# Optimization experiments

Measured on AMD Instinct MI355X. Metric: run time of the kernel, lower is better.

The kernel has to match this reference:

```python
import jax, jax.numpy as jnp
import numpy as np

N_NODES = 100000
N_EDGES = 3200000
N_GRAPHS = 1024
DIMS = [14, 64, 64, 32, 2]


def _add_self_loops(edge_index, n):
    loop = jnp.arange(n, dtype=edge_index.dtype)
    src = jnp.concatenate([edge_index[0], loop])
    dst = jnp.concatenate([edge_index[1], loop])
    return src, dst


def _gcn_norm(src, dst, n):
    # symmetric normalization D^{-1/2} (A+I) D^{-1/2}; degree from target nodes
    deg = jax.ops.segment_sum(jnp.ones_like(dst, dtype=jnp.float32), dst, num_segments=n)
    dinv = jnp.where(deg > 0, jax.lax.rsqrt(deg), 0.0)
    return dinv[src] * dinv[dst]


def gcn_conv(x, W, b, src, dst, norm, n):
    h = x @ W                          # [N, out] small GEMM first (out <= in here is fine either way)
    msg = h[src] * norm[:, None]       # gather + edge scale  [E+N, out]
    agg = jax.ops.segment_sum(msg, dst, num_segments=n)  # scatter-add
    return agg + b


def setup_inputs() -> dict:
    key = jax.random.key(0)
    ks = jax.random.split(key, 16)
    x = jax.random.normal(ks[0], (N_NODES, DIMS[0]), dtype=jnp.float32)
    edge_index = jax.random.randint(ks[1], (2, N_EDGES), 0, N_NODES, dtype=jnp.int64)
    batch = jnp.sort(jax.random.randint(ks[2], (N_NODES,), 0, N_GRAPHS, dtype=jnp.int64))
    params = {}
    for i in range(4):
        fan_in = DIMS[i]
        params[f"W{i+1}"] = jax.random.normal(ks[3 + 2 * i], (DIMS[i], DIMS[i + 1]), dtype=jnp.float32) / np.sqrt(fan_in)
        params[f"b{i+1}"] = jnp.zeros((DIMS[i + 1],), dtype=jnp.float32)
    return {"x": x, "edge_index": edge_index, "batch": batch, **params}


def reference(x, edge_index, batch, W1, b1, W2, b2, W3, b3, W4, b4):
    n = x.shape[0]
    src, dst = _add_self_loops(edge_index, n)
    norm = _gcn_norm(src, dst, n)
    h = jax.nn.relu(gcn_conv(x, W1, b1, src, dst, norm, n))
    # dropout layers are identity in eval mode
    h = jax.nn.relu(gcn_conv(h, W2, b2, src, dst, norm, n))
    h = jax.nn.relu(gcn_conv(h, W3, b3, src, dst, norm, n))
    h = gcn_conv(h, W4, b4, src, dst, norm, n)
    pooled = jax.ops.segment_max(h, batch, num_segments=N_GRAPHS)  # [G, C]
    pooled = jnp.where(jnp.isfinite(pooled), pooled, 0.0)  # guard empty graphs
    return jax.nn.log_softmax(pooled, axis=-1)
```

## Files before the change

### kernel.cpp

```cpp
#include <hip/hip_runtime.h>
#include <math.h>

#define WAVE 64
#define BINSHIFT 9
#define NPB 512
#define NBLK 512
#define MAXBINS 256
#define BINCAP 17408

typedef int vint4 __attribute__((ext_vector_type(4)));
typedef unsigned int uint;
typedef unsigned char uchar;
typedef __attribute__((ext_vector_type(8))) short bf16x8;
typedef __attribute__((ext_vector_type(4))) float f32x4;

__device__ inline float bflo(uint u) { return __uint_as_float(u << 16); }
__device__ inline float bfhi(uint u) { return __uint_as_float(u & 0xffff0000u); }
__device__ inline uint pack_bf2(float a, float b) {
    uint ua = __float_as_uint(a), ub = __float_as_uint(b);
    uint ra = (ua + 0x7fffu + ((ua >> 16) & 1u)) >> 16;
    uint rb = (ub + 0x7fffu + ((ub >> 16) & 1u)) & 0xffff0000u;
    return ra | rb;
}
__device__ inline ushort bf16r(float f) {
    uint u = __float_as_uint(f);
    u += 0x7fffu + ((u >> 16) & 1u);
    return (ushort)(u >> 16);
}


#if defined(__HIP_DEVICE_COMPILE__) && __has_builtin(__builtin_amdgcn_cvt_pk_f32_fp8) && __has_builtin(__builtin_amdgcn_cvt_pk_fp8_f32)
#define FP8_HW 1
#else
#define FP8_HW 0
#endif

__device__ inline uint fp8_enc1(float x) {
    float cx = fminf(fmaxf(x, -448.f), 448.f);
    uint s = (__float_as_uint(cx) >> 24) & 0x80u;
    float ax = fabsf(cx);
    uint r = __float_as_uint(ax);
    uint keep = r >> 20;
    uint rem = r & 0xFFFFFu;
    keep += (rem > 0x80000u || (rem == 0x80000u && (keep & 1u))) ? 1u : 0u;
    int em = (int)keep - (120 << 3);
    uint sub = (uint)__float2int_rn(ax * 512.f);
    uint v = (ax >= 0.015625f) ? (uint)(em > 0x7E ? 0x7E : em) : sub;
    return s | v;
}
__device__ inline float fp8_dec1(uint b) {
    uint s = (b & 0x80u) << 24;
    uint em = b & 0x7Fu;
    float mag = (em >= 8u)
        ? __uint_as_float((((em >> 3) + 120u) << 23) | ((em & 7u) << 20))
        : (float)em * 0.001953125f;
    return __uint_as_float(s | __float_as_uint(mag));
}

__device__ inline uint fp8x4_enc(float a0, float a1, float a2, float a3) {
#if FP8_HW
    int v = __builtin_amdgcn_cvt_pk_fp8_f32(a0, a1, 0, 0);
    v     = __builtin_amdgcn_cvt_pk_fp8_f32(a2, a3, v, 1);
    return (uint)v;
#else
    return fp8_enc1(a0) | (fp8_enc1(a1) << 8) | (fp8_enc1(a2) << 16) | (fp8_enc1(a3) << 24);
#endif
}
__device__ inline void fp8x4_dec(uint u, float& a0, float& a1, float& a2, float& a3) {
#if FP8_HW
    auto lo = __builtin_amdgcn_cvt_pk_f32_fp8((int)u, 0);
    auto hi = __builtin_amdgcn_cvt_pk_f32_fp8((int)u, 1);
    a0 = lo[0]; a1 = lo[1]; a2 = hi[0]; a3 = hi[1];
#else
    a0 = fp8_dec1(u & 0xffu); a1 = fp8_dec1((u >> 8) & 0xffu);
    a2 = fp8_dec1((u >> 16) & 0xffu); a3 = fp8_dec1(u >> 24);
#endif
}


__global__ __launch_bounds__(1024) void hist_k(const int* __restrict__ ei, int* __restrict__ counts,
                                               int E, int nbins) {
    __shared__ int scnt[MAXBINS];
    int t = threadIdx.x, b = blockIdx.x;
    if (t < nbins) scnt[t] = 0;
    __syncthreads();
    int nq  = E >> 2;
    int qpb = (nq + NBLK - 1) / NBLK;
    int q0 = b * qpb, q1 = min(q0 + qpb, nq);
    for (int q = q0 + t; q < q1; q += 1024) {
        vint4 d4 = __builtin_nontemporal_load(reinterpret_cast<const vint4*>(ei + E + q * 4));
        atomicAdd(&scnt[d4.x >> BINSHIFT], 1);
        atomicAdd(&scnt[d4.y >> BINSHIFT], 1);
        atomicAdd(&scnt[d4.z >> BINSHIFT], 1);
        atomicAdd(&scnt[d4.w >> BINSHIFT], 1);
    }
    if (b == NBLK - 1 && t == 0)
        for (int e = (E & ~3); e < E; ++e) atomicAdd(&scnt[ei[E + e] >> BINSHIFT], 1);
    __syncthreads();
    if (t < nbins) counts[b * nbins + t] = scnt[t];
}


__global__ __launch_bounds__(NBLK) void scan_k(const int* __restrict__ counts, int* __restrict__ prefix,
                                               int* __restrict__ totals, const int* __restrict__ batch,
                                               int* __restrict__ gstart, ushort* __restrict__ padX,
                                               uint* __restrict__ pad8, int nbins, int N, int Gn) {
    __shared__ int sm[NBLK];
    int bin = blockIdx.x, t = threadIdx.x;
    int v = counts[t * nbins + bin];
    sm[t] = v;
    __syncthreads();
    for (int off = 1; off < NBLK; off <<= 1) {
        int x = (t >= off) ? sm[t - off] : 0;
        __syncthreads();
        sm[t] += x;
        __syncthreads();
    }
    prefix[t * nbins + bin] = sm[t] - v;
    if (t == NBLK - 1) totals[bin] = sm[t];
    int gtid = bin * NBLK + t;
    if (gtid < N) {
        int bi = batch[gtid];
        int bp = (gtid == 0) ? -1 : batch[gtid - 1];
        for (int g = bp + 1; g <= bi; ++g) gstart[g] = gtid;
        if (gtid == N - 1)
            for (int g = bi + 1; g <= Gn; ++g) gstart[g] = N;
    }
    if (gtid < 128) padX[gtid] = 0;
    if (gtid < 64)  pad8[gtid] = 0;
}


__global__ __launch_bounds__(1024) void place_k(const int* __restrict__ ei, const int* __restrict__ prefix,
                                                int* __restrict__ binned, int E, int nbins) {
    __shared__ int soff[MAXBINS];
    int t = threadIdx.x, b = blockIdx.x;
    if (t < nbins) soff[t] = prefix[b * nbins + t];
    __syncthreads();
    int nq  = E >> 2;
    int qpb = (nq + NBLK - 1) / NBLK;
    int q0 = b * qpb, q1 = min(q0 + qpb, nq);
    for (int q = q0 + t; q < q1; q += 1024) {
        vint4 s4 = __builtin_nontemporal_load(reinterpret_cast<const vint4*>(ei + q * 4));
        vint4 d4 = __builtin_nontemporal_load(reinterpret_cast<const vint4*>(ei + E + q * 4));
        int bb, p;
        bb = d4.x >> BINSHIFT; p = atomicAdd(&soff[bb], 1);
        if (p < BINCAP) binned[bb * BINCAP + p] = ((d4.x & (NPB - 1)) << 17) | s4.x;
        bb = d4.y >> BINSHIFT; p = atomicAdd(&soff[bb], 1);
        if (p < BINCAP) binned[bb * BINCAP + p] = ((d4.y & (NPB - 1)) << 17) | s4.y;
        bb = d4.z >> BINSHIFT; p = atomicAdd(&soff[bb], 1);
        if (p < BINCAP) binned[bb * BINCAP + p] = ((d4.z & (NPB - 1)) << 17) | s4.z;
        bb = d4.w >> BINSHIFT; p = atomicAdd(&soff[bb], 1);
        if (p < BINCAP) binned[bb * BINCAP + p] = ((d4.w & (NPB - 1)) << 17) | s4.w;
    }
    if (b == NBLK - 1 && t == 0) {
        for (int e = (E & ~3); e < E; ++e) {
            int d = ei[E + e], bb = d >> BINSHIFT;
            int p = atomicAdd(&soff[bb], 1);
            if (p < BINCAP) binned[bb * BINCAP + p] = ((d & (NPB - 1)) << 17) | ei[e];
        }
    }
}


__global__ __launch_bounds__(1024) void bin_sort_k(
    const int* __restrict__ totals, const int* __restrict__ binned, const float* __restrict__ x,
    int* __restrict__ csr, int* __restrict__ deg, int* __restrict__ rowstart,
    float* __restrict__ dinv_g, ushort* __restrict__ xs0b, int N) {
    __shared__ int scnt[NPB];
    __shared__ int sscan[NPB];
    __shared__ int sfill[NPB];
    int bin = blockIdx.x;
    int t   = threadIdx.x;
    int total = totals[bin];
    if (total > BINCAP) total = BINCAP;
    if (t < NPB) { scnt[t] = 0; sfill[t] = 0; }
    __syncthreads();
    const int* gsrc = binned + bin * BINCAP;
    for (int i = t; i < total; i += 1024) atomicAdd(&scnt[gsrc[i] >> 17], 1);
    __syncthreads();
    if (t < NPB) sscan[t] = scnt[t];
    __syncthreads();
    for (int off = 1; off < NPB; off <<= 1) {
        int a = (t < NPB && t >= off) ? sscan[t - off] : 0;
        __syncthreads();
        if (t < NPB) sscan[t] += a;
        __syncthreads();
    }
    int obase = bin * BINCAP;
    for (int i = t; i < total; i += 1024) {
        int rec = gsrc[i], n = rec >> 17;
        int r = atomicAdd(&sfill[n], 1);
        csr[obase + (sscan[n] - scnt[n]) + r] = rec & 0x1FFFF;
    }
    if (t < NPB) {
        int node = (bin << BINSHIFT) + t;
        if (node < N) {
            int c = scnt[t];
            deg[node]      = c;
            rowstart[node] = obase + sscan[t] - c;
            dinv_g[node]   = rsqrtf((float)(c + 1));
        }
    }
    int base = bin << BINSHIFT;
    for (int i = t; i < NPB * 8; i += 1024) {
        int nloc = i >> 3, c2 = i & 7;
        int node = base + nloc;
        if (node < N) {
            float di = rsqrtf((float)(scnt[nloc] + 1));
            int c0 = c2 * 2, c1 = c0 + 1;
            float a = (c0 < 14) ? x[node * 14 + c0] * di : 0.f;
            float b = (c1 < 14) ? x[node * 14 + c1] * di : 0.f;
            reinterpret_cast<uint*>(xs0b)[node * 8 + c2] = pack_bf2(a, b);
        }
    }
}


__global__ __launch_bounds__(256) void agg12_k(
    const ushort* __restrict__ xs, const int* __restrict__ deg, const int* __restrict__ rowstart,
    const int* __restrict__ csr, const float* __restrict__ dinv,
    const float* __restrict__ W1, const float* __restrict__ b1,
    uchar* __restrict__ h1f8, int N) {
    const int G = 4;
    __shared__ float sW1[14 * 64];
    __shared__ float sB1[64];
    int t = threadIdx.x;
    for (int i = t; i < 14 * 64; i += 256) sW1[i] = W1[i];
    if (t < 64) sB1[t] = b1[t];
    __syncthreads();
    int tid  = blockIdx.x * 256 + t;
    int lane = t & (WAVE - 1);
    int wave = tid >> 6;
    int node = wave * (WAVE / G) + lane / G;
    int cg   = lane % G;
    if (node >= N) return;
    int s = rowstart[node];
    int e = s + deg[node];
    float4 acc = {0.f, 0.f, 0.f, 0.f};
    for (int j = s; j < e; j += G) {
        int es = (j + cg < e) ? csr[j + cg] : -1;
#pragma unroll
        for (int k = 0; k < G; ++k) {
            int sk = __shfl(es, k, G);
            uint2 u = *reinterpret_cast<const uint2*>(xs + (long)sk * 16 + (cg << 2));
            acc.x += bflo(u.x); acc.y += bfhi(u.x);
            acc.z += bflo(u.y); acc.w += bfhi(u.y);
        }
    }
    {
        uint2 u = *reinterpret_cast<const uint2*>(xs + (long)node * 16 + (cg << 2));
        acc.x += bflo(u.x); acc.y += bfhi(u.x);
        acc.z += bflo(u.y); acc.w += bfhi(u.y);
    }
    float di = dinv[node];
    float r0 = acc.x * di, r1 = acc.y * di, r2 = acc.z * di, r3 = acc.w * di;
    float rr[16];
#pragma unroll
    for (int k = 0; k < 4; ++k) {
        rr[4 * k + 0] = __shfl(r0, k, G);
        rr[4 * k + 1] = __shfl(r1, k, G);
        rr[4 * k + 2] = __shfl(r2, k, G);
        rr[4 * k + 3] = __shfl(r3, k, G);
    }
    int ob = cg << 4;
    float a[16];
#pragma unroll
    for (int o = 0; o < 16; ++o) a[o] = sB1[ob + o];
#pragma unroll
    for (int c = 0; c < 14; ++c) {
        float rc = rr[c];
#pragma unroll
        for (int o = 0; o < 16; ++o) a[o] += rc * sW1[c * 64 + ob + o];
    }
    uint* orow = reinterpret_cast<uint*>(h1f8 + (long)node * 64 + ob);
#pragma unroll
    for (int o = 0; o < 16; o += 4) {
        float x0 = fmaxf(a[o + 0], 0.f) * di;
        float x1 = fmaxf(a[o + 1], 0.f) * di;
        float x2 = fmaxf(a[o + 2], 0.f) * di;
        float x3 = fmaxf(a[o + 3], 0.f) * di;
        orow[o >> 2] = fp8x4_enc(x0, x1, x2, x3);
    }
}


template <int CO, int G>
__global__ __launch_bounds__(256) void agg2_k(
    const uint* __restrict__ xs, ushort* __restrict__ out,
    const int* __restrict__ deg, const int* __restrict__ rowstart, const int* __restrict__ csr,
    const float* __restrict__ dinv, int N) {
    int tid  = blockIdx.x * blockDim.x + threadIdx.x;
    int lane = threadIdx.x & (WAVE - 1);
    int wave = tid >> 6;
    int node = wave * (WAVE / G) + lane / G;
    int cg   = lane % G;
    if (node >= N) return;
    int s = rowstart[node];
    int e = s + deg[node];
    float4 acc = {0.f, 0.f, 0.f, 0.f};
    for (int j = s; j < e; j += G) {
        int es = (j + cg < e) ? csr[j + cg] : -1;
#pragma unroll
        for (int k = 0; k < G; ++k) {
            int sk = __shfl(es, k, G);
            uint u = xs[(long)sk * G + cg];
            float a0, a1, a2, a3;
            fp8x4_dec(u, a0, a1, a2, a3);
            acc.x += a0; acc.y += a1; acc.z += a2; acc.w += a3;
        }
    }
    {
        uint u = xs[(long)node * G + cg];
        float a0, a1, a2, a3;
        fp8x4_dec(u, a0, a1, a2, a3);
        acc.x += a0; acc.y += a1; acc.z += a2; acc.w += a3;
    }
    float di = dinv[node];
    uint2 o;
    o.x = pack_bf2(acc.x * di, acc.y * di);
    o.y = pack_bf2(acc.z * di, acc.w * di);
    *reinterpret_cast<uint2*>(out + (long)node * CO + (cg << 2)) = o;
}


#define GW 72

__global__ __launch_bounds__(256) void gemm23_k(
    const ushort* __restrict__ inb, const float* __restrict__ W2, const float* __restrict__ b2,
    const float* __restrict__ W3, const float* __restrict__ dinv,
    uchar* __restrict__ outp, int N) {
    __shared__ ushort sW2t[64 * GW];
    __shared__ ushort sW3t[32 * GW];
    __shared__ float  sB2[64];
    __shared__ ushort sH[4][16 * GW];
    __shared__ uchar  sO[4][16 * 32];
    int t = threadIdx.x;
    for (int i = t; i < 64 * 64; i += 256) {
        int k = i >> 6, n = i & 63;
        sW2t[n * GW + k] = bf16r(W2[k * 64 + n]);
    }
    for (int i = t; i < 64 * 32; i += 256) {
        int k = i >> 5, n = i & 31;
        sW3t[n * GW + k] = bf16r(W3[k * 32 + n]);
    }
    if (t < 64) sB2[t] = b2[t];
    __syncthreads();

    int w    = t >> 6;
    int lane = t & 63;
    int m16  = lane & 15;
    int q    = lane >> 4;
    int base = blockIdx.x * 64 + w * 16;

    bf16x8 a0 = *reinterpret_cast<const bf16x8*>(inb + (long)(base + m16) * 64 + q * 8);
    bf16x8 a1 = *reinterpret_cast<const bf16x8*>(inb + (long)(base + m16) * 64 + 32 + q * 8);

    f32x4 acc1[4];
#pragma unroll
    for (int nt = 0; nt < 4; ++nt) {
        f32x4 c = {0.f, 0.f, 0.f, 0.f};
        bf16x8 b0 = *reinterpret_cast<const bf16x8*>(&sW2t[(nt * 16 + m16) * GW + q * 8]);
        bf16x8 b1 = *reinterpret_cast<const bf16x8*>(&sW2t[(nt * 16 + m16) * GW + 32 + q * 8]);
        c = __builtin_amdgcn_mfma_f32_16x16x32_bf16(a0, b0, c, 0, 0, 0);
        c = __builtin_amdgcn_mfma_f32_16x16x32_bf16(a1, b1, c, 0, 0, 0);
        acc1[nt] = c;
    }
    ushort* hT = sH[w];
#pragma unroll
    for (int nt = 0; nt < 4; ++nt) {
        float bb = sB2[nt * 16 + m16];
#pragma unroll
        for (int r = 0; r < 4; ++r) {
            float h = fmaxf(acc1[nt][r] + bb, 0.f);
            hT[(q * 4 + r) * GW + nt * 16 + m16] = bf16r(h);
        }
    }
    __syncthreads();
    bf16x8 a20 = *reinterpret_cast<const bf16x8*>(&hT[m16 * GW + q * 8]);
    bf16x8 a21 = *reinterpret_cast<const bf16x8*>(&hT[m16 * GW + 32 + q * 8]);
    f32x4 acc2[2];
#pragma unroll
    for (int nt = 0; nt < 2; ++nt) {
        f32x4 c = {0.f, 0.f, 0.f, 0.f};
        bf16x8 b0 = *reinterpret_cast<const bf16x8*>(&sW3t[(nt * 16 + m16) * GW + q * 8]);
        bf16x8 b1 = *reinterpret_cast<const bf16x8*>(&sW3t[(nt * 16 + m16) * GW + 32 + q * 8]);
        c = __builtin_amdgcn_mfma_f32_16x16x32_bf16(a20, b0, c, 0, 0, 0);
        c = __builtin_amdgcn_mfma_f32_16x16x32_bf16(a21, b1, c, 0, 0, 0);
        acc2[nt] = c;
    }
    uchar* oT = sO[w];
#pragma unroll
    for (int r = 0; r < 4; ++r) {
        int m = q * 4 + r;
        float di = dinv[min(base + m, N - 1)];
#pragma unroll
        for (int nt = 0; nt < 2; ++nt)
            oT[m * 32 + nt * 16 + m16] = (uchar)fp8_enc1(acc2[nt][r] * di);
    }
    __syncthreads();
    const uint* src = reinterpret_cast<const uint*>(oT);
    uint* dst = reinterpret_cast<uint*>(outp + (long)base * 32);
    dst[lane] = src[lane];
    dst[lane + 64] = src[lane + 64];
}


__global__ __launch_bounds__(256) void agg34_k(
    const uint* __restrict__ xs, const int* __restrict__ deg, const int* __restrict__ rowstart,
    const int* __restrict__ csr, const float* __restrict__ dinv, const float* __restrict__ b3,
    const float* __restrict__ W4, ushort* __restrict__ usb, int N) {
    const int G = 8;
    __shared__ float sW4[64];
    __shared__ float sB3[32];
    int t = threadIdx.x;
    if (t < 64) sW4[t] = W4[t];
    if (t < 32) sB3[t] = b3[t];
    __syncthreads();
    int tid  = blockIdx.x * 256 + t;
    int lane = t & (WAVE - 1);
    int wave = tid >> 6;
    int node = wave * (WAVE / G) + lane / G;
    int cg   = lane % G;
    if (node >= N) return;
    int s = rowstart[node];
    int e = s + deg[node];
    float4 acc = {0.f, 0.f, 0.f, 0.f};
    for (int j = s; j < e; j += G) {
        int es = (j + cg < e) ? csr[j + cg] : -1;
#pragma unroll
        for (int k = 0; k < G; ++k) {
            int sk = __shfl(es, k, G);
            uint u = xs[(long)sk * G + cg];
            float a0, a1, a2, a3;
            fp8x4_dec(u, a0, a1, a2, a3);
            acc.x += a0; acc.y += a1; acc.z += a2; acc.w += a3;
        }
    }
    {
        uint u = xs[(long)node * G + cg];
        float a0, a1, a2, a3;
        fp8x4_dec(u, a0, a1, a2, a3);
        acc.x += a0; acc.y += a1; acc.z += a2; acc.w += a3;
    }
    float di = dinv[node];
    int cb = cg << 2;
    float h0 = fmaxf(acc.x * di + sB3[cb + 0], 0.f);
    float h1 = fmaxf(acc.y * di + sB3[cb + 1], 0.f);
    float h2 = fmaxf(acc.z * di + sB3[cb + 2], 0.f);
    float h3 = fmaxf(acc.w * di + sB3[cb + 3], 0.f);
    float p0 = h0 * sW4[(cb + 0) * 2 + 0] + h1 * sW4[(cb + 1) * 2 + 0]
             + h2 * sW4[(cb + 2) * 2 + 0] + h3 * sW4[(cb + 3) * 2 + 0];
    float p1 = h0 * sW4[(cb + 0) * 2 + 1] + h1 * sW4[(cb + 1) * 2 + 1]
             + h2 * sW4[(cb + 2) * 2 + 1] + h3 * sW4[(cb + 3) * 2 + 1];
#pragma unroll
    for (int o = 4; o >= 1; o >>= 1) {
        p0 += __shfl_xor(p0, o, WAVE);
        p1 += __shfl_xor(p1, o, WAVE);
    }
    if (cg == 0)
        reinterpret_cast<uint*>(usb)[node] = pack_bf2(p0 * di, p1 * di);
}


#define PG 16

__global__ __launch_bounds__(256) void agg4_k(
    const ushort* __restrict__ xs, const int* __restrict__ deg, const int* __restrict__ rowstart,
    const int* __restrict__ csr, const float* __restrict__ dinv, const float* __restrict__ bias,
    float* __restrict__ nodeout, int N) {
    int tid  = blockIdx.x * 256 + threadIdx.x;
    int lane = threadIdx.x & (WAVE - 1);
    int wave = tid >> 6;
    int node = wave * (WAVE / PG) + lane / PG;
    int l    = lane % PG;
    if (node >= N) return;
    int s = rowstart[node];
    int e = s + deg[node];
    float ax = 0.f, ay = 0.f;
    for (int j = s + l; j < e; j += PG) {
        int es = csr[j];
        uint u = *reinterpret_cast<const uint*>(xs + (long)es * 2);
        ax += bflo(u); ay += bfhi(u);
    }
#pragma unroll
    for (int o = PG / 2; o >= 1; o >>= 1) {
        ax += __shfl_xor(ax, o, WAVE);
        ay += __shfl_xor(ay, o, WAVE);
    }
    if (l == 0) {
        uint u = *reinterpret_cast<const uint*>(xs + (long)node * 2);
        ax += bflo(u); ay += bfhi(u);
        float di = dinv[node];
        float2 r;
        r.x = ax * di + bias[0];
        r.y = ay * di + bias[1];
        *reinterpret_cast<float2*>(nodeout + (long)node * 2) = r;
    }
}


__global__ __launch_bounds__(256) void pool_g_k(
    const float* __restrict__ nodeout, const int* __restrict__ gstart,
    float* __restrict__ out, int Gn) {
    int wave = (blockIdx.x * 256 + threadIdx.x) >> 6;
    int lane = threadIdx.x & (WAVE - 1);
    if (wave >= Gn) return;
    int s = gstart[wave], e = gstart[wave + 1];
    float ax = -INFINITY, ay = -INFINITY;
    for (int i = s + lane; i < e; i += WAVE) {
        float2 v = *reinterpret_cast<const float2*>(nodeout + (long)i * 2);
        ax = fmaxf(ax, v.x); ay = fmaxf(ay, v.y);
    }
#pragma unroll
    for (int o = 32; o >= 1; o >>= 1) {
        ax = fmaxf(ax, __shfl_xor(ax, o, WAVE));
        ay = fmaxf(ay, __shfl_xor(ay, o, WAVE));
    }
    if (lane == 0) {
        if (!isfinite(ax)) ax = 0.f;
        if (!isfinite(ay)) ay = 0.f;
        float m = fmaxf(ax, ay);
        float lse = m + logf(expf(ax - m) + expf(ay - m));
        out[wave * 2 + 0] = ax - lse;
        out[wave * 2 + 1] = ay - lse;
    }
}


static inline int agg_blocks(int N, int G) {
    long waves = ((long)N + (WAVE / G) - 1) / (WAVE / G);
    return (int)((waves * WAVE + 255) / 256);
}

extern "C" void kernel_launch(void* const* d_in, const int* in_sizes, int n_in,
                              void* d_out, int out_size, void* d_ws, size_t ws_size,
                              hipStream_t stream) {
    const float* x     = (const float*)d_in[0];
    const int*   ei    = (const int*)d_in[1];
    const int*   batch = (const int*)d_in[2];
    const float* W1 = (const float*)d_in[3];
    const float* b1 = (const float*)d_in[4];
    const float* W2 = (const float*)d_in[5];
    const float* b2 = (const float*)d_in[6];
    const float* W3 = (const float*)d_in[7];
    const float* b3 = (const float*)d_in[8];
    const float* W4 = (const float*)d_in[9];
    const float* b4 = (const float*)d_in[10];
    float* out = (float*)d_out;

    int N  = in_sizes[0] / 14;
    int E  = in_sizes[1] / 2;
    int Gn = out_size / 2;
    int nbins = (N + NPB - 1) >> BINSHIFT;

    char* ws = (char*)d_ws;
    size_t off = 0;
    auto alloc = [&](size_t bytes) -> char* {
        char* p = ws + off;
        off = (off + bytes + 255) & ~(size_t)255;
        return p;
    };
    int*    deg      = (int*)alloc((size_t)N * 4);
    int*    rowstart = (int*)alloc((size_t)N * 4);
    float*  dinv     = (float*)alloc((size_t)N * 4);
    int*    gstart   = (int*)alloc((size_t)(Gn + 1) * 4);
    int*    counts   = (int*)alloc((size_t)NBLK * nbins * 4);
    int*    prefix   = (int*)alloc((size_t)NBLK * nbins * 4);
    int*    totals   = (int*)alloc((size_t)nbins * 4);
    int*    csr      = (int*)alloc((size_t)nbins * BINCAP * 4);
    int*    binned   = (int*)alloc((size_t)nbins * BINCAP * 4);
    ushort* padX     = (ushort*)alloc(256 + (size_t)N * 16 * 2);
    ushort* xs0b     = padX + 128;
    uint*   pad8     = (uint*)alloc(256 + (size_t)(N + 64) * 64);
    uchar*  h1f8     = (uchar*)(pad8 + 64);
    ushort* Bf1b     = (ushort*)alloc((size_t)(N + 64) * 64 * 2);
    uchar*  tsf8     = h1f8;
    ushort* usb      = xs0b;
    float*  nodeout  = (float*)binned;
    (void)ws_size; (void)n_in;

    hist_k<<<NBLK, 1024, 0, stream>>>(ei, counts, E, nbins);
    scan_k<<<nbins, NBLK, 0, stream>>>(counts, prefix, totals, batch, gstart, padX, pad8, nbins, N, Gn);
    place_k<<<NBLK, 1024, 0, stream>>>(ei, prefix, binned, E, nbins);
    bin_sort_k<<<nbins, 1024, 0, stream>>>(totals, binned, x, csr, deg, rowstart, dinv, xs0b, N);

    agg12_k<<<agg_blocks(N, 4), 256, 0, stream>>>(xs0b, deg, rowstart, csr, dinv, W1, b1, h1f8, N);

    agg2_k<64, 16><<<agg_blocks(N, 16), 256, 0, stream>>>((const uint*)h1f8, Bf1b, deg, rowstart, csr, dinv, N);

    gemm23_k<<<(N + 63) / 64, 256, 0, stream>>>(Bf1b, W2, b2, W3, dinv, tsf8, N);

    agg34_k<<<agg_blocks(N, 8), 256, 0, stream>>>((const uint*)tsf8, deg, rowstart, csr, dinv, b3, W4, usb, N);

    agg4_k<<<agg_blocks(N, PG), 256, 0, stream>>>(usb, deg, rowstart, csr, dinv, b4, nodeout, N);
    pool_g_k<<<(Gn * WAVE + 255) / 256, 256, 0, stream>>>(nodeout, gstart, out, Gn);
}
```

Before: 268.6 us.

## Fuse layer-2 aggregation with the W2/W3 MFMA GEMMs in one kernel

Merges the layer-2 gather/aggregate kernel and the following two-stage bf16 MFMA GEMM kernel into one 1024-thread block kernel. Each block aggregates 64 nodes into shared memory, then 16 waves split the W2 and W3 tiles. This drops the bf16 intermediate buffer's global write and read and one launch. In exchange it uses larger blocks with more shared memory, which can reduce occupancy for the latency-bound gather phase and idles half the waves during the W3 step. The output moves to a separate padded fp8 buffer because it can no longer alias the input.

```diff
diff --git a/kernel.cpp b/kernel.cpp
--- a/kernel.cpp
+++ b/kernel.cpp
@@ -104,7 +104,8 @@
 __global__ __launch_bounds__(NBLK) void scan_k(const int* __restrict__ counts, int* __restrict__ prefix,
                                                int* __restrict__ totals, const int* __restrict__ batch,
                                                int* __restrict__ gstart, ushort* __restrict__ padX,
-                                               uint* __restrict__ pad8, int nbins, int N, int Gn) {
+                                               uint* __restrict__ pad8, uint* __restrict__ pad8b,
+                                               int nbins, int N, int Gn) {
     __shared__ int sm[NBLK];
     int bin = blockIdx.x, t = threadIdx.x;
     int v = counts[t * nbins + bin];
@@ -127,7 +128,7 @@
             for (int g = bi + 1; g <= Gn; ++g) gstart[g] = N;
     }
     if (gtid < 128) padX[gtid] = 0;
-    if (gtid < 64)  pad8[gtid] = 0;
+    if (gtid < 64)  { pad8[gtid] = 0; pad8b[gtid] = 0; }
 }
 
 
@@ -285,124 +286,111 @@
 }
 
 
-template <int CO, int G>
-__global__ __launch_bounds__(256) void agg2_k(
-    const uint* __restrict__ xs, ushort* __restrict__ out,
-    const int* __restrict__ deg, const int* __restrict__ rowstart, const int* __restrict__ csr,
-    const float* __restrict__ dinv, int N) {
-    int tid  = blockIdx.x * blockDim.x + threadIdx.x;
-    int lane = threadIdx.x & (WAVE - 1);
-    int wave = tid >> 6;
-    int node = wave * (WAVE / G) + lane / G;
-    int cg   = lane % G;
-    if (node >= N) return;
-    int s = rowstart[node];
-    int e = s + deg[node];
-    float4 acc = {0.f, 0.f, 0.f, 0.f};
-    for (int j = s; j < e; j += G) {
-        int es = (j + cg < e) ? csr[j + cg] : -1;
-#pragma unroll
-        for (int k = 0; k < G; ++k) {
-            int sk = __shfl(es, k, G);
-            uint u = xs[(long)sk * G + cg];
-            float a0, a1, a2, a3;
-            fp8x4_dec(u, a0, a1, a2, a3);
-            acc.x += a0; acc.y += a1; acc.z += a2; acc.w += a3;
-        }
-    }
-    {
-        uint u = xs[(long)node * G + cg];
-        float a0, a1, a2, a3;
-        fp8x4_dec(u, a0, a1, a2, a3);
-        acc.x += a0; acc.y += a1; acc.z += a2; acc.w += a3;
-    }
-    float di = dinv[node];
-    uint2 o;
-    o.x = pack_bf2(acc.x * di, acc.y * di);
-    o.y = pack_bf2(acc.z * di, acc.w * di);
-    *reinterpret_cast<uint2*>(out + (long)node * CO + (cg << 2)) = o;
-}
-
-
 #define GW 72
 
-__global__ __launch_bounds__(256) void gemm23_k(
-    const ushort* __restrict__ inb, const float* __restrict__ W2, const float* __restrict__ b2,
-    const float* __restrict__ W3, const float* __restrict__ dinv,
+__global__ __launch_bounds__(1024) void agg23_k(
+    const uint* __restrict__ xs, const int* __restrict__ deg, const int* __restrict__ rowstart,
+    const int* __restrict__ csr, const float* __restrict__ dinv,
+    const float* __restrict__ W2, const float* __restrict__ b2, const float* __restrict__ W3,
     uchar* __restrict__ outp, int N) {
     __shared__ ushort sW2t[64 * GW];
     __shared__ ushort sW3t[32 * GW];
     __shared__ float  sB2[64];
+    __shared__ ushort sA[64 * GW];
     __shared__ ushort sH[4][16 * GW];
-    __shared__ uchar  sO[4][16 * 32];
+    __shared__ uchar  sO[64 * 32];
     int t = threadIdx.x;
-    for (int i = t; i < 64 * 64; i += 256) {
+    for (int i = t; i < 64 * 64; i += 1024) {
         int k = i >> 6, n = i & 63;
         sW2t[n * GW + k] = bf16r(W2[k * 64 + n]);
     }
-    for (int i = t; i < 64 * 32; i += 256) {
+    for (int i = t; i < 64 * 32; i += 1024) {
         int k = i >> 5, n = i & 31;
         sW3t[n * GW + k] = bf16r(W3[k * 32 + n]);
     }
     if (t < 64) sB2[t] = b2[t];
-    __syncthreads();
 
     int w    = t >> 6;
     int lane = t & 63;
-    int m16  = lane & 15;
-    int q    = lane >> 4;
-    int base = blockIdx.x * 64 + w * 16;
-
-    bf16x8 a0 = *reinterpret_cast<const bf16x8*>(inb + (long)(base + m16) * 64 + q * 8);
-    bf16x8 a1 = *reinterpret_cast<const bf16x8*>(inb + (long)(base + m16) * 64 + 32 + q * 8);
-
-    f32x4 acc1[4];
-#pragma unroll
-    for (int nt = 0; nt < 4; ++nt) {
+    int nl   = w * 4 + (lane >> 4);
+    int cg   = lane & 15;
+    int base = blockIdx.x * 64;
+    int node = base + nl;
+
+    float4 acc = {0.f, 0.f, 0.f, 0.f};
+    if (node < N) {
+        int s = rowstart[node];
+        int e = s + deg[node];
+        for (int j = s; j < e; j += 16) {
+            int es = (j + cg < e) ? csr[j + cg] : -1;
+#pragma unroll
+            for (int k = 0; k < 16; ++k) {
+                int sk = __shfl(es, k, 16);
+                uint u = xs[(long)sk * 16 + cg];
+                float a0, a1, a2, a3;
+                fp8x4_dec(u, a0, a1, a2, a3);
+                acc.x += a0; acc.y += a1; acc.z += a2; acc.w += a3;
+            }
+        }
+        {
+            uint u = xs[(long)node * 16 + cg];
+            float a0, a1, a2, a3;
+            fp8x4_dec(u, a0, a1, a2, a3);
+            acc.x += a0; acc.y += a1; acc.z += a2; acc.w += a3;
+        }
+        float di = dinv[node];
+        acc.x *= di; acc.y *= di; acc.z *= di; acc.w *= di;
+    }
+    {
+        uint2 o;
+        o.x = pack_bf2(acc.x, acc.y);
+        o.y = pack_bf2(acc.z, acc.w);
+        *reinterpret_cast<uint2*>(&sA[nl * GW + (cg << 2)]) = o;
+    }
+    __syncthreads();
+
+    int rt  = w & 3, ct = w >> 2;
+    int m16 = lane & 15;
+    int q   = lane >> 4;
+    bf16x8 a0 = *reinterpret_cast<const bf16x8*>(&sA[(rt * 16 + m16) * GW + q * 8]);
+    bf16x8 a1 = *reinterpret_cast<const bf16x8*>(&sA[(rt * 16 + m16) * GW + 32 + q * 8]);
+    {
         f32x4 c = {0.f, 0.f, 0.f, 0.f};
-        bf16x8 b0 = *reinterpret_cast<const bf16x8*>(&sW2t[(nt * 16 + m16) * GW + q * 8]);
-        bf16x8 b1 = *reinterpret_cast<const bf16x8*>(&sW2t[(nt * 16 + m16) * GW + 32 + q * 8]);
+        bf16x8 b0 = *reinterpret_cast<const bf16x8*>(&sW2t[(ct * 16 + m16) * GW + q * 8]);
+        bf16x8 b1 = *reinterpret_cast<const bf16x8*>(&sW2t[(ct * 16 + m16) * GW + 32 + q * 8]);
         c = __builtin_amdgcn_mfma_f32_16x16x32_bf16(a0, b0, c, 0, 0, 0);
         c = __builtin_amdgcn_mfma_f32_16x16x32_bf16(a1, b1, c, 0, 0, 0);
-        acc1[nt] = c;
-    }
-    ushort* hT = sH[w];
-#pragma unroll
-    for (int nt = 0; nt < 4; ++nt) {
-        float bb = sB2[nt * 16 + m16];
+        float bb = sB2[ct * 16 + m16];
+        ushort* hT = sH[rt];
 #pragma unroll
         for (int r = 0; r < 4; ++r) {
-            float h = fmaxf(acc1[nt][r] + bb, 0.f);
-            hT[(q * 4 + r) * GW + nt * 16 + m16] = bf16r(h);
-        }
-    }
-    __syncthreads();
-    bf16x8 a20 = *reinterpret_cast<const bf16x8*>(&hT[m16 * GW + q * 8]);
-    bf16x8 a21 = *reinterpret_cast<const bf16x8*>(&hT[m16 * GW + 32 + q * 8]);
-    f32x4 acc2[2];
-#pragma unroll
-    for (int nt = 0; nt < 2; ++nt) {
+            float h = fmaxf(c[r] + bb, 0.f);
+            hT[(q * 4 + r) * GW + ct * 16 + m16] = bf16r(h);
+        }
+    }
+    __syncthreads();
+    if (ct < 2) {
+        ushort* hT = sH[rt];
+        bf16x8 a20 = *reinterpret_cast<const bf16x8*>(&hT[m16 * GW + q * 8]);
+        bf16x8 a21 = *reinterpret_cast<const bf16x8*>(&hT[m16 * GW + 32 + q * 8]);
         f32x4 c = {0.f, 0.f, 0.f, 0.f};
-        bf16x8 b0 = *reinterpret_cast<const bf16x8*>(&sW3t[(nt * 16 + m16) * GW + q * 8]);
-        bf16x8 b1 = *reinterpret_cast<const bf16x8*>(&sW3t[(nt * 16 + m16) * GW + 32 + q * 8]);
+        bf16x8 b0 = *reinterpret_cast<const bf16x8*>(&sW3t[(ct * 16 + m16) * GW + q * 8]);
+        bf16x8 b1 = *reinterpret_cast<const bf16x8*>(&sW3t[(ct * 16 + m16) * GW + 32 + q * 8]);
         c = __builtin_amdgcn_mfma_f32_16x16x32_bf16(a20, b0, c, 0, 0, 0);
         c = __builtin_amdgcn_mfma_f32_16x16x32_bf16(a21, b1, c, 0, 0, 0);
-        acc2[nt] = c;
-    }
-    uchar* oT = sO[w];
-#pragma unroll
-    for (int r = 0; r < 4; ++r) {
-        int m = q * 4 + r;
-        float di = dinv[min(base + m, N - 1)];
-#pragma unroll
-        for (int nt = 0; nt < 2; ++nt)
-            oT[m * 32 + nt * 16 + m16] = (uchar)fp8_enc1(acc2[nt][r] * di);
-    }
-    __syncthreads();
-    const uint* src = reinterpret_cast<const uint*>(oT);
-    uint* dst = reinterpret_cast<uint*>(outp + (long)base * 32);
-    dst[lane] = src[lane];
-    dst[lane + 64] = src[lane + 64];
+#pragma unroll
+        for (int r = 0; r < 4; ++r) {
+            int m = rt * 16 + q * 4 + r;
+            float di = dinv[min(base + m, N - 1)];
+            sO[m * 32 + ct * 16 + m16] = (uchar)fp8_enc1(c[r] * di);
+        }
+    }
+    __syncthreads();
+    if (t < 512) {
+        const uint* src = reinterpret_cast<const uint*>(sO);
+        uint* dst = reinterpret_cast<uint*>(outp + (long)base * 32);
+        dst[t] = src[t];
+    }
 }
 
 
@@ -572,24 +560,22 @@
     int*    binned   = (int*)alloc((size_t)nbins * BINCAP * 4);
     ushort* padX     = (ushort*)alloc(256 + (size_t)N * 16 * 2);
     ushort* xs0b     = padX + 128;
-    uint*   pad8     = (uint*)alloc(256 + (size_t)(N + 64) * 64);
+    uint*   pad8     = (uint*)alloc(256 + (size_t)N * 64);
     uchar*  h1f8     = (uchar*)(pad8 + 64);
-    ushort* Bf1b     = (ushort*)alloc((size_t)(N + 64) * 64 * 2);
-    uchar*  tsf8     = h1f8;
+    uint*   pad8b    = (uint*)alloc(256 + (size_t)(N + 64) * 32);
+    uchar*  tsf8     = (uchar*)(pad8b + 64);
     ushort* usb      = xs0b;
     float*  nodeout  = (float*)binned;
     (void)ws_size; (void)n_in;
 
     hist_k<<<NBLK, 1024, 0, stream>>>(ei, counts, E, nbins);
-    scan_k<<<nbins, NBLK, 0, stream>>>(counts, prefix, totals, batch, gstart, padX, pad8, nbins, N, Gn);
+    scan_k<<<nbins, NBLK, 0, stream>>>(counts, prefix, totals, batch, gstart, padX, pad8, pad8b, nbins, N, Gn);
     place_k<<<NBLK, 1024, 0, stream>>>(ei, prefix, binned, E, nbins);
     bin_sort_k<<<nbins, 1024, 0, stream>>>(totals, binned, x, csr, deg, rowstart, dinv, xs0b, N);
 
     agg12_k<<<agg_blocks(N, 4), 256, 0, stream>>>(xs0b, deg, rowstart, csr, dinv, W1, b1, h1f8, N);
 
-    agg2_k<64, 16><<<agg_blocks(N, 16), 256, 0, stream>>>((const uint*)h1f8, Bf1b, deg, rowstart, csr, dinv, N);
-
-    gemm23_k<<<(N + 63) / 64, 256, 0, stream>>>(Bf1b, W2, b2, W3, dinv, tsf8, N);
+    agg23_k<<<(N + 63) / 64, 1024, 0, stream>>>((const uint*)h1f8, deg, rowstart, csr, dinv, W2, b2, W3, tsf8, N);
 
     agg34_k<<<agg_blocks(N, 8), 256, 0, stream>>>((const uint*)tsf8, deg, rowstart, csr, dinv, b3, W4, usb, N);
 
```

Result: slower. 285.6 us (+6.3%).

## Split layer-2 aggregation into two 32-channel halves with nontemporal CSR loads

Applied to the files above, without the earlier changes.

The 64-channel fp8 hidden features after layer 1 are now stored as two separate 32-byte-per-node arrays, and the layer-2 aggregation runs as two launches that each gather one half into the matching channel offset of the bf16 output. Each gather pass touches a smaller feature table (about 3.2 MB instead of 6.4 MB), so it should stay more resident in L2/LLC. The cost is that the CSR index stream and the edge loop are traversed twice. CSR index loads in all aggregation kernels also switch to nontemporal loads to reduce cache pollution from the streamed indices.

```diff
diff --git a/kernel.cpp b/kernel.cpp
--- a/kernel.cpp
+++ b/kernel.cpp
@@ -104,7 +104,8 @@
 __global__ __launch_bounds__(NBLK) void scan_k(const int* __restrict__ counts, int* __restrict__ prefix,
                                                int* __restrict__ totals, const int* __restrict__ batch,
                                                int* __restrict__ gstart, ushort* __restrict__ padX,
-                                               uint* __restrict__ pad8, int nbins, int N, int Gn) {
+                                               uint* __restrict__ pad8a, uint* __restrict__ pad8b,
+                                               int nbins, int N, int Gn) {
     __shared__ int sm[NBLK];
     int bin = blockIdx.x, t = threadIdx.x;
     int v = counts[t * nbins + bin];
@@ -127,7 +128,7 @@
             for (int g = bi + 1; g <= Gn; ++g) gstart[g] = N;
     }
     if (gtid < 128) padX[gtid] = 0;
-    if (gtid < 64)  pad8[gtid] = 0;
+    if (gtid < 64)  { pad8a[gtid] = 0; pad8b[gtid] = 0; }
 }
 
 
@@ -221,7 +222,7 @@
     const ushort* __restrict__ xs, const int* __restrict__ deg, const int* __restrict__ rowstart,
     const int* __restrict__ csr, const float* __restrict__ dinv,
     const float* __restrict__ W1, const float* __restrict__ b1,
-    uchar* __restrict__ h1f8, int N) {
+    uchar* __restrict__ h1a, uchar* __restrict__ h1b, int N) {
     const int G = 4;
     __shared__ float sW1[14 * 64];
     __shared__ float sB1[64];
@@ -239,7 +240,7 @@
     int e = s + deg[node];
     float4 acc = {0.f, 0.f, 0.f, 0.f};
     for (int j = s; j < e; j += G) {
-        int es = (j + cg < e) ? csr[j + cg] : -1;
+        int es = (j + cg < e) ? __builtin_nontemporal_load(csr + j + cg) : -1;
 #pragma unroll
         for (int k = 0; k < G; ++k) {
             int sk = __shfl(es, k, G);
@@ -273,7 +274,9 @@
 #pragma unroll
         for (int o = 0; o < 16; ++o) a[o] += rc * sW1[c * 64 + ob + o];
     }
-    uint* orow = reinterpret_cast<uint*>(h1f8 + (long)node * 64 + ob);
+    uint* orow = (cg < 2)
+        ? reinterpret_cast<uint*>(h1a + (long)node * 32 + (cg << 4))
+        : reinterpret_cast<uint*>(h1b + (long)node * 32 + ((cg - 2) << 4));
 #pragma unroll
     for (int o = 0; o < 16; o += 4) {
         float x0 = fmaxf(a[o + 0], 0.f) * di;
@@ -285,11 +288,11 @@
 }
 
 
-template <int CO, int G>
-__global__ __launch_bounds__(256) void agg2_k(
+__global__ __launch_bounds__(256) void agg2h_k(
     const uint* __restrict__ xs, ushort* __restrict__ out,
     const int* __restrict__ deg, const int* __restrict__ rowstart, const int* __restrict__ csr,
-    const float* __restrict__ dinv, int N) {
+    const float* __restrict__ dinv, int chanoff, int N) {
+    const int G = 8;
     int tid  = blockIdx.x * blockDim.x + threadIdx.x;
     int lane = threadIdx.x & (WAVE - 1);
     int wave = tid >> 6;
@@ -300,18 +303,18 @@
     int e = s + deg[node];
     float4 acc = {0.f, 0.f, 0.f, 0.f};
     for (int j = s; j < e; j += G) {
-        int es = (j + cg < e) ? csr[j + cg] : -1;
+        int es = (j + cg < e) ? __builtin_nontemporal_load(csr + j + cg) : -1;
 #pragma unroll
         for (int k = 0; k < G; ++k) {
             int sk = __shfl(es, k, G);
-            uint u = xs[(long)sk * G + cg];
+            uint u = xs[(long)sk * 8 + cg];
             float a0, a1, a2, a3;
             fp8x4_dec(u, a0, a1, a2, a3);
             acc.x += a0; acc.y += a1; acc.z += a2; acc.w += a3;
         }
     }
     {
-        uint u = xs[(long)node * G + cg];
+        uint u = xs[(long)node * 8 + cg];
         float a0, a1, a2, a3;
         fp8x4_dec(u, a0, a1, a2, a3);
         acc.x += a0; acc.y += a1; acc.z += a2; acc.w += a3;
@@ -320,7 +323,7 @@
     uint2 o;
     o.x = pack_bf2(acc.x * di, acc.y * di);
     o.y = pack_bf2(acc.z * di, acc.w * di);
-    *reinterpret_cast<uint2*>(out + (long)node * CO + (cg << 2)) = o;
+    *reinterpret_cast<uint2*>(out + (long)node * 64 + chanoff + (cg << 2)) = o;
 }
 
 
@@ -427,7 +430,7 @@
     int e = s + deg[node];
     float4 acc = {0.f, 0.f, 0.f, 0.f};
     for (int j = s; j < e; j += G) {
-        int es = (j + cg < e) ? csr[j + cg] : -1;
+        int es = (j + cg < e) ? __builtin_nontemporal_load(csr + j + cg) : -1;
 #pragma unroll
         for (int k = 0; k < G; ++k) {
             int sk = __shfl(es, k, G);
@@ -479,7 +482,7 @@
     int e = s + deg[node];
     float ax = 0.f, ay = 0.f;
     for (int j = s + l; j < e; j += PG) {
-        int es = csr[j];
+        int es = __builtin_nontemporal_load(csr + j);
         uint u = *reinterpret_cast<const uint*>(xs + (long)es * 2);
         ax += bflo(u); ay += bfhi(u);
     }
@@ -572,22 +575,25 @@
     int*    binned   = (int*)alloc((size_t)nbins * BINCAP * 4);
     ushort* padX     = (ushort*)alloc(256 + (size_t)N * 16 * 2);
     ushort* xs0b     = padX + 128;
-    uint*   pad8     = (uint*)alloc(256 + (size_t)(N + 64) * 64);
-    uchar*  h1f8     = (uchar*)(pad8 + 64);
+    uint*   pad8a    = (uint*)alloc(256 + (size_t)(N + 64) * 32);
+    uchar*  h1a      = (uchar*)(pad8a + 64);
+    uint*   pad8b    = (uint*)alloc(256 + (size_t)N * 32);
+    uchar*  h1b      = (uchar*)(pad8b + 64);
     ushort* Bf1b     = (ushort*)alloc((size_t)(N + 64) * 64 * 2);
-    uchar*  tsf8     = h1f8;
+    uchar*  tsf8     = h1a;
     ushort* usb      = xs0b;
     float*  nodeout  = (float*)binned;
     (void)ws_size; (void)n_in;
 
     hist_k<<<NBLK, 1024, 0, stream>>>(ei, counts, E, nbins);
-    scan_k<<<nbins, NBLK, 0, stream>>>(counts, prefix, totals, batch, gstart, padX, pad8, nbins, N, Gn);
+    scan_k<<<nbins, NBLK, 0, stream>>>(counts, prefix, totals, batch, gstart, padX, pad8a, pad8b, nbins, N, Gn);
     place_k<<<NBLK, 1024, 0, stream>>>(ei, prefix, binned, E, nbins);
     bin_sort_k<<<nbins, 1024, 0, stream>>>(totals, binned, x, csr, deg, rowstart, dinv, xs0b, N);
 
-    agg12_k<<<agg_blocks(N, 4), 256, 0, stream>>>(xs0b, deg, rowstart, csr, dinv, W1, b1, h1f8, N);
-
-    agg2_k<64, 16><<<agg_blocks(N, 16), 256, 0, stream>>>((const uint*)h1f8, Bf1b, deg, rowstart, csr, dinv, N);
+    agg12_k<<<agg_blocks(N, 4), 256, 0, stream>>>(xs0b, deg, rowstart, csr, dinv, W1, b1, h1a, h1b, N);
+
+    agg2h_k<<<agg_blocks(N, 8), 256, 0, stream>>>((const uint*)h1a, Bf1b, deg, rowstart, csr, dinv, 0, N);
+    agg2h_k<<<agg_blocks(N, 8), 256, 0, stream>>>((const uint*)h1b, Bf1b, deg, rowstart, csr, dinv, 32, N);
 
     gemm23_k<<<(N + 63) / 64, 256, 0, stream>>>(Bf1b, W2, b2, W3, dinv, tsf8, N);
 
```

New measurement: 315.9 us. 1.18x slower.

## Split edges across lanes with full-row loads and butterfly reduction in aggregation kernels

Applied to the files above, without the earlier changes.

The three CSR aggregation kernels change from having each lane own a channel slice of every neighbour row to having each lane own a subset of edges and load whole rows with wide 16-byte loads. Partial sums are then combined with xor-shuffle butterfly reductions that halve the channel count at each step. This removes the per-edge index broadcast shuffles and the narrow per-lane gathers, so each lane issues fewer, larger memory requests. In exchange it needs many more accumulator registers per thread (64 floats in agg2), which may lower occupancy, and agg2 moves from 16 to 8 lanes per node.

```diff
diff --git a/kernel.cpp b/kernel.cpp
--- a/kernel.cpp
+++ b/kernel.cpp
@@ -237,32 +237,31 @@
     if (node >= N) return;
     int s = rowstart[node];
     int e = s + deg[node];
-    float4 acc = {0.f, 0.f, 0.f, 0.f};
-    for (int j = s; j < e; j += G) {
-        int es = (j + cg < e) ? csr[j + cg] : -1;
-#pragma unroll
-        for (int k = 0; k < G; ++k) {
-            int sk = __shfl(es, k, G);
-            uint2 u = *reinterpret_cast<const uint2*>(xs + (long)sk * 16 + (cg << 2));
-            acc.x += bflo(u.x); acc.y += bfhi(u.x);
-            acc.z += bflo(u.y); acc.w += bfhi(u.y);
-        }
-    }
-    {
-        uint2 u = *reinterpret_cast<const uint2*>(xs + (long)node * 16 + (cg << 2));
-        acc.x += bflo(u.x); acc.y += bfhi(u.x);
-        acc.z += bflo(u.y); acc.w += bfhi(u.y);
-    }
+    float acc[16];
+#pragma unroll
+    for (int o = 0; o < 16; ++o) acc[o] = 0.f;
+    auto addrow = [&](long r) {
+        const uint4* p = reinterpret_cast<const uint4*>(xs + r * 16);
+        uint4 u0 = p[0], u1 = p[1];
+        acc[0]  += bflo(u0.x); acc[1]  += bfhi(u0.x);
+        acc[2]  += bflo(u0.y); acc[3]  += bfhi(u0.y);
+        acc[4]  += bflo(u0.z); acc[5]  += bfhi(u0.z);
+        acc[6]  += bflo(u0.w); acc[7]  += bfhi(u0.w);
+        acc[8]  += bflo(u1.x); acc[9]  += bfhi(u1.x);
+        acc[10] += bflo(u1.y); acc[11] += bfhi(u1.y);
+        acc[12] += bflo(u1.z); acc[13] += bfhi(u1.z);
+        acc[14] += bflo(u1.w); acc[15] += bfhi(u1.w);
+    };
+    if (cg == 0) addrow(node);
+    for (int j = s + cg; j < e; j += G) addrow(csr[j]);
+#pragma unroll
+    for (int m = 1; m < G; m <<= 1)
+#pragma unroll
+        for (int o = 0; o < 16; ++o) acc[o] += __shfl_xor(acc[o], m, G);
     float di = dinv[node];
-    float r0 = acc.x * di, r1 = acc.y * di, r2 = acc.z * di, r3 = acc.w * di;
     float rr[16];
 #pragma unroll
-    for (int k = 0; k < 4; ++k) {
-        rr[4 * k + 0] = __shfl(r0, k, G);
-        rr[4 * k + 1] = __shfl(r1, k, G);
-        rr[4 * k + 2] = __shfl(r2, k, G);
-        rr[4 * k + 3] = __shfl(r3, k, G);
-    }
+    for (int o = 0; o < 16; ++o) rr[o] = acc[o] * di;
     int ob = cg << 4;
     float a[16];
 #pragma unroll
@@ -273,24 +272,31 @@
 #pragma unroll
         for (int o = 0; o < 16; ++o) a[o] += rc * sW1[c * 64 + ob + o];
     }
-    uint* orow = reinterpret_cast<uint*>(h1f8 + (long)node * 64 + ob);
-#pragma unroll
-    for (int o = 0; o < 16; o += 4) {
-        float x0 = fmaxf(a[o + 0], 0.f) * di;
-        float x1 = fmaxf(a[o + 1], 0.f) * di;
-        float x2 = fmaxf(a[o + 2], 0.f) * di;
-        float x3 = fmaxf(a[o + 3], 0.f) * di;
-        orow[o >> 2] = fp8x4_enc(x0, x1, x2, x3);
-    }
-}
-
-
-template <int CO, int G>
+    uint4 ov;
+    {
+        float x0 = fmaxf(a[0], 0.f) * di,  x1 = fmaxf(a[1], 0.f) * di;
+        float x2 = fmaxf(a[2], 0.f) * di,  x3 = fmaxf(a[3], 0.f) * di;
+        ov.x = fp8x4_enc(x0, x1, x2, x3);
+        x0 = fmaxf(a[4], 0.f) * di;  x1 = fmaxf(a[5], 0.f) * di;
+        x2 = fmaxf(a[6], 0.f) * di;  x3 = fmaxf(a[7], 0.f) * di;
+        ov.y = fp8x4_enc(x0, x1, x2, x3);
+        x0 = fmaxf(a[8], 0.f) * di;  x1 = fmaxf(a[9], 0.f) * di;
+        x2 = fmaxf(a[10], 0.f) * di; x3 = fmaxf(a[11], 0.f) * di;
+        ov.z = fp8x4_enc(x0, x1, x2, x3);
+        x0 = fmaxf(a[12], 0.f) * di; x1 = fmaxf(a[13], 0.f) * di;
+        x2 = fmaxf(a[14], 0.f) * di; x3 = fmaxf(a[15], 0.f) * di;
+        ov.w = fp8x4_enc(x0, x1, x2, x3);
+    }
+    *reinterpret_cast<uint4*>(h1f8 + (long)node * 64 + ob) = ov;
+}
+
+
 __global__ __launch_bounds__(256) void agg2_k(
-    const uint* __restrict__ xs, ushort* __restrict__ out,
+    const uchar* __restrict__ xs, ushort* __restrict__ out,
     const int* __restrict__ deg, const int* __restrict__ rowstart, const int* __restrict__ csr,
     const float* __restrict__ dinv, int N) {
-    int tid  = blockIdx.x * blockDim.x + threadIdx.x;
+    const int G = 8;
+    int tid  = blockIdx.x * 256 + threadIdx.x;
     int lane = threadIdx.x & (WAVE - 1);
     int wave = tid >> 6;
     int node = wave * (WAVE / G) + lane / G;
@@ -298,29 +304,58 @@
     if (node >= N) return;
     int s = rowstart[node];
     int e = s + deg[node];
-    float4 acc = {0.f, 0.f, 0.f, 0.f};
-    for (int j = s; j < e; j += G) {
-        int es = (j + cg < e) ? csr[j + cg] : -1;
-#pragma unroll
-        for (int k = 0; k < G; ++k) {
-            int sk = __shfl(es, k, G);
-            uint u = xs[(long)sk * G + cg];
+    float acc[64];
+#pragma unroll
+    for (int o = 0; o < 64; ++o) acc[o] = 0.f;
+    auto addrow = [&](long r) {
+        const uint4* p = reinterpret_cast<const uint4*>(xs + r * 64);
+        uint4 q0 = p[0], q1 = p[1], q2 = p[2], q3 = p[3];
+        uint w[16] = {q0.x, q0.y, q0.z, q0.w, q1.x, q1.y, q1.z, q1.w,
+                      q2.x, q2.y, q2.z, q2.w, q3.x, q3.y, q3.z, q3.w};
+#pragma unroll
+        for (int o = 0; o < 16; ++o) {
             float a0, a1, a2, a3;
-            fp8x4_dec(u, a0, a1, a2, a3);
-            acc.x += a0; acc.y += a1; acc.z += a2; acc.w += a3;
-        }
-    }
+            fp8x4_dec(w[o], a0, a1, a2, a3);
+            acc[4 * o] += a0; acc[4 * o + 1] += a1;
+            acc[4 * o + 2] += a2; acc[4 * o + 3] += a3;
+        }
+    };
+    if (cg == 0) addrow(node);
+    for (int j = s + cg; j < e; j += G) addrow(csr[j]);
     {
-        uint u = xs[(long)node * G + cg];
-        float a0, a1, a2, a3;
-        fp8x4_dec(u, a0, a1, a2, a3);
-        acc.x += a0; acc.y += a1; acc.z += a2; acc.w += a3;
+        bool sel = (cg & 4) != 0;
+#pragma unroll
+        for (int o = 0; o < 32; ++o) {
+            float keep = sel ? acc[o + 32] : acc[o];
+            float give = sel ? acc[o] : acc[o + 32];
+            acc[o] = keep + __shfl_xor(give, 4, G);
+        }
+    }
+    {
+        bool sel = (cg & 2) != 0;
+#pragma unroll
+        for (int o = 0; o < 16; ++o) {
+            float keep = sel ? acc[o + 16] : acc[o];
+            float give = sel ? acc[o] : acc[o + 16];
+            acc[o] = keep + __shfl_xor(give, 2, G);
+        }
+    }
+    {
+        bool sel = (cg & 1) != 0;
+#pragma unroll
+        for (int o = 0; o < 8; ++o) {
+            float keep = sel ? acc[o + 8] : acc[o];
+            float give = sel ? acc[o] : acc[o + 8];
+            acc[o] = keep + __shfl_xor(give, 1, G);
+        }
     }
     float di = dinv[node];
-    uint2 o;
-    o.x = pack_bf2(acc.x * di, acc.y * di);
-    o.y = pack_bf2(acc.z * di, acc.w * di);
-    *reinterpret_cast<uint2*>(out + (long)node * CO + (cg << 2)) = o;
+    uint4 ov;
+    ov.x = pack_bf2(acc[0] * di, acc[1] * di);
+    ov.y = pack_bf2(acc[2] * di, acc[3] * di);
+    ov.z = pack_bf2(acc[4] * di, acc[5] * di);
+    ov.w = pack_bf2(acc[6] * di, acc[7] * di);
+    *reinterpret_cast<uint4*>(out + (long)node * 64 + (cg << 3)) = ov;
 }
 
 
@@ -407,7 +442,7 @@
 
 
 __global__ __launch_bounds__(256) void agg34_k(
-    const uint* __restrict__ xs, const int* __restrict__ deg, const int* __restrict__ rowstart,
+    const uchar* __restrict__ xs, const int* __restrict__ deg, const int* __restrict__ rowstart,
     const int* __restrict__ csr, const float* __restrict__ dinv, const float* __restrict__ b3,
     const float* __restrict__ W4, ushort* __restrict__ usb, int N) {
     const int G = 8;
@@ -425,30 +460,56 @@
     if (node >= N) return;
     int s = rowstart[node];
     int e = s + deg[node];
-    float4 acc = {0.f, 0.f, 0.f, 0.f};
-    for (int j = s; j < e; j += G) {
-        int es = (j + cg < e) ? csr[j + cg] : -1;
-#pragma unroll
-        for (int k = 0; k < G; ++k) {
-            int sk = __shfl(es, k, G);
-            uint u = xs[(long)sk * G + cg];
+    float acc[32];
+#pragma unroll
+    for (int o = 0; o < 32; ++o) acc[o] = 0.f;
+    auto addrow = [&](long r) {
+        const uint4* p = reinterpret_cast<const uint4*>(xs + r * 32);
+        uint4 q0 = p[0], q1 = p[1];
+        uint w[8] = {q0.x, q0.y, q0.z, q0.w, q1.x, q1.y, q1.z, q1.w};
+#pragma unroll
+        for (int o = 0; o < 8; ++o) {
             float a0, a1, a2, a3;
-            fp8x4_dec(u, a0, a1, a2, a3);
-            acc.x += a0; acc.y += a1; acc.z += a2; acc.w += a3;
-        }
-    }
+            fp8x4_dec(w[o], a0, a1, a2, a3);
+            acc[4 * o] += a0; acc[4 * o + 1] += a1;
+            acc[4 * o + 2] += a2; acc[4 * o + 3] += a3;
+        }
+    };
+    if (cg == 0) addrow(node);
+    for (int j = s + cg; j < e; j += G) addrow(csr[j]);
     {
-        uint u = xs[(long)node * G + cg];
-        float a0, a1, a2, a3;
-        fp8x4_dec(u, a0, a1, a2, a3);
-        acc.x += a0; acc.y += a1; acc.z += a2; acc.w += a3;
+        bool sel = (cg & 4) != 0;
+#pragma unroll
+        for (int o = 0; o < 16; ++o) {
+            float keep = sel ? acc[o + 16] : acc[o];
+            float give = sel ? acc[o] : acc[o + 16];
+            acc[o] = keep + __shfl_xor(give, 4, G);
+        }
+    }
+    {
+        bool sel = (cg & 2) != 0;
+#pragma unroll
+        for (int o = 0; o < 8; ++o) {
+            float keep = sel ? acc[o + 8] : acc[o];
+            float give = sel ? acc[o] : acc[o + 8];
+            acc[o] = keep + __shfl_xor(give, 2, G);
+        }
+    }
+    {
+        bool sel = (cg & 1) != 0;
+#pragma unroll
+        for (int o = 0; o < 4; ++o) {
+            float keep = sel ? acc[o + 4] : acc[o];
+            float give = sel ? acc[o] : acc[o + 4];
+            acc[o] = keep + __shfl_xor(give, 1, G);
+        }
     }
     float di = dinv[node];
     int cb = cg << 2;
-    float h0 = fmaxf(acc.x * di + sB3[cb + 0], 0.f);
-    float h1 = fmaxf(acc.y * di + sB3[cb + 1], 0.f);
-    float h2 = fmaxf(acc.z * di + sB3[cb + 2], 0.f);
-    float h3 = fmaxf(acc.w * di + sB3[cb + 3], 0.f);
+    float h0 = fmaxf(acc[0] * di + sB3[cb + 0], 0.f);
+    float h1 = fmaxf(acc[1] * di + sB3[cb + 1], 0.f);
+    float h2 = fmaxf(acc[2] * di + sB3[cb + 2], 0.f);
+    float h3 = fmaxf(acc[3] * di + sB3[cb + 3], 0.f);
     float p0 = h0 * sW4[(cb + 0) * 2 + 0] + h1 * sW4[(cb + 1) * 2 + 0]
              + h2 * sW4[(cb + 2) * 2 + 0] + h3 * sW4[(cb + 3) * 2 + 0];
     float p1 = h0 * sW4[(cb + 0) * 2 + 1] + h1 * sW4[(cb + 1) * 2 + 1]
@@ -587,11 +648,11 @@
 
     agg12_k<<<agg_blocks(N, 4), 256, 0, stream>>>(xs0b, deg, rowstart, csr, dinv, W1, b1, h1f8, N);
 
-    agg2_k<64, 16><<<agg_blocks(N, 16), 256, 0, stream>>>((const uint*)h1f8, Bf1b, deg, rowstart, csr, dinv, N);
+    agg2_k<<<agg_blocks(N, 8), 256, 0, stream>>>(h1f8, Bf1b, deg, rowstart, csr, dinv, N);
 
     gemm23_k<<<(N + 63) / 64, 256, 0, stream>>>(Bf1b, W2, b2, W3, dinv, tsf8, N);
 
-    agg34_k<<<agg_blocks(N, 8), 256, 0, stream>>>((const uint*)tsf8, deg, rowstart, csr, dinv, b3, W4, usb, N);
+    agg34_k<<<agg_blocks(N, 8), 256, 0, stream>>>(tsf8, deg, rowstart, csr, dinv, b3, W4, usb, N);
 
     agg4_k<<<agg_blocks(N, PG), 256, 0, stream>>>(usb, deg, rowstart, csr, dinv, b4, nodeout, N);
     pool_g_k<<<(Gn * WAVE + 255) / 256, 256, 0, stream>>>(nodeout, gstart, out, Gn);
```

Result: slower. 286.5 us (+6.6%).
